# Kernel tuning notes

Hardware: AMD Instinct MI355X
Metric: run time of the kernel (lower is better)

## Reference

```python
import jax, jax.numpy as jnp
import numpy as np

B, D, C = 4096, 4096, 1024


def setup_inputs() -> dict:
    key = jax.random.key(0)
    kx, kw = jax.random.split(key)
    x = jax.random.normal(kx, (B, D), dtype=jnp.float32)
    # kaiming_normal_ with nonlinearity='relu': std = sqrt(2 / fan_in)
    W = jax.random.normal(kw, (C, D), dtype=jnp.float32) * jnp.sqrt(2.0 / D)
    return {"x": x, "W": W}


def reference(x, W):
    # Original: -( (x[:, :, None] - W.T[None, :, :])**2 ).mean(axis=1)
    d = x.shape[1]
    x_sq = jnp.sum(x * x, axis=1, keepdims=True)        # [B, 1]
    w_sq = jnp.sum(W * W, axis=1)[None, :]              # [1, C]
    cross = jnp.einsum('bd,cd->bc', x, W)               # [B, C] tensor-core GEMM
    return -(x_sq - 2.0 * cross + w_sq) / d
```

## Files before the change

kernel.cpp:

```cpp
#include <hip/hip_runtime.h>
#include <hip/hip_bf16.h>


typedef float f32x4 __attribute__((ext_vector_type(4)));
typedef float f32x2 __attribute__((ext_vector_type(2)));
typedef float f32x16 __attribute__((ext_vector_type(16)));
typedef int i32x4 __attribute__((ext_vector_type(4)));
typedef int i32x8 __attribute__((ext_vector_type(8)));

#define BDIM 4096
#define DDIM 4096
#define CDIM 1024
#define TM 128
#define TN 128
#define BK 64
#define NIT (DDIM / BK)
#define SCALE 32.0f
#define INV_SS (1.0f/1024.0f)

#define WAITV(N) asm volatile("s_waitcnt vmcnt(" #N ")" ::: "memory")

__global__ __launch_bounds__(256) void cvt_rowsq(
    const float* __restrict__ x, const float* __restrict__ W,
    unsigned char* __restrict__ xb, unsigned char* __restrict__ wb,
    float* __restrict__ xsq, float* __restrict__ wsq)
{
    const int lane = threadIdx.x & 63;
    const int row = blockIdx.x * 4 + (threadIdx.x >> 6);

    const float* src;
    unsigned char* dst;
    float* sq;
    if (row < BDIM) {
        src = x + (size_t)row * DDIM;
        dst = xb + (size_t)row * DDIM;
        sq = xsq + row;
    } else {
        int r = row - BDIM;
        src = W + (size_t)r * DDIM;
        dst = wb + (size_t)r * DDIM;
        sq = wsq + r;
    }

    const float4* s4 = (const float4*)src;
    unsigned int* d4 = (unsigned int*)dst;
    float a = 0.f;
    #pragma unroll
    for (int s = 0; s < DDIM / 4 / 64; ++s) {
        float4 f = s4[lane + 64 * s];
        a += f.x * f.x + f.y * f.y + f.z * f.z + f.w * f.w;
        unsigned int p = 0;
        p = __builtin_amdgcn_cvt_pk_fp8_f32(f.x * SCALE, f.y * SCALE, p, false);
        p = __builtin_amdgcn_cvt_pk_fp8_f32(f.z * SCALE, f.w * SCALE, p, true);
        d4[lane + 64 * s] = p;
    }
    #pragma unroll
    for (int off = 32; off > 0; off >>= 1) a += __shfl_down(a, off);
    if (lane == 0) *sq = a;
}


__device__ __forceinline__ i32x8 cat8(i32x4 lo, i32x4 hi) {
    return __builtin_shufflevector(lo, hi, 0, 1, 2, 3, 4, 5, 6, 7);
}

#define MXMFMA(A, Bv, C)                                                  \
    __builtin_amdgcn_mfma_scale_f32_32x32x64_f8f6f4(                      \
        (A), (Bv), (C), 0, 0, 0, 0x7F7F7F7F, 0, 0x7F7F7F7F)

#define GLOAD16(gp, lp)                                                   \
    __builtin_amdgcn_global_load_lds(                                     \
        (const __attribute__((address_space(1))) void*)(gp),              \
        (__attribute__((address_space(3))) void*)(lp), 16, 0, 0)

__global__ __launch_bounds__(256) void gemm_eucl(
    const unsigned char* __restrict__ xb,
    const unsigned char* __restrict__ wb,
    const float* __restrict__ xsq, const float* __restrict__ wsq,
    float* __restrict__ out)
{
    __shared__ unsigned char sm[4 * 3 * 8192];

    const int tid = threadIdx.x;
    const int lane = tid & 63;
    const int w = tid >> 6;
    const int wr = w >> 1;
    const int wc = w & 1;
    const int bm = blockIdx.x * TM;
    const int bn = blockIdx.y * TN;

    unsigned char* wbase = sm + w * 24576;

    const int lr = lane >> 2;
    const int schunk = ((lane & 3) ^ ((lane >> 3) & 3)) * 16;
    const unsigned char* gA[4];
    const unsigned char* gB[4];
    #pragma unroll
    for (int i = 0; i < 4; ++i) {
        gA[i] = xb + (size_t)(bm + wr * 64 + 16 * i + lr) * DDIM + schunk;
        gB[i] = wb + (size_t)(bn + wc * 64 + 16 * i + lr) * DDIM + schunk;
    }

#define STAGE(q, t)                                                       \
    do {                                                                  \
        _Pragma("unroll")                                                 \
        for (int i = 0; i < 4; ++i) {                                     \
            GLOAD16(gA[i] + (t) * BK, wbase + (q) * 8192 + i * 1024);     \
            GLOAD16(gB[i] + (t) * BK, wbase + (q) * 8192 + 4096 + i * 1024); \
        }                                                                 \
    } while (0)

    const int s_rd = ((lane & 31) >> 1) & 3;
    const int c0s = ((lane >> 5) * 2) ^ s_rd;
    const unsigned char* aR0 = wbase + (lane & 31) * 64 + c0s * 16;
    const unsigned char* aR1 = wbase + (lane & 31) * 64 + (c0s ^ 1) * 16;
    const unsigned char* bR0 = aR0 + 4096;
    const unsigned char* bR1 = aR1 + 4096;

    f32x16 acc[4] = {};

#define COMPUTE(qo)                                                       \
    do {                                                                  \
        i32x8 fb0 = cat8(*(const i32x4*)(bR0 + (qo)),                     \
                         *(const i32x4*)(bR1 + (qo)));                    \
        i32x8 fb1 = cat8(*(const i32x4*)(bR0 + (qo) + 2048),              \
                         *(const i32x4*)(bR1 + (qo) + 2048));             \
        i32x8 fa0 = cat8(*(const i32x4*)(aR0 + (qo)),                     \
                         *(const i32x4*)(aR1 + (qo)));                    \
        i32x8 fa1 = cat8(*(const i32x4*)(aR0 + (qo) + 2048),              \
                         *(const i32x4*)(aR1 + (qo) + 2048));             \
        __builtin_amdgcn_s_setprio(1);                                    \
        acc[0] = MXMFMA(fa0, fb0, acc[0]);                                \
        acc[1] = MXMFMA(fa0, fb1, acc[1]);                                \
        acc[2] = MXMFMA(fa1, fb0, acc[2]);                                \
        acc[3] = MXMFMA(fa1, fb1, acc[3]);                                \
        __builtin_amdgcn_s_setprio(0);                                    \
    } while (0)

    STAGE(0, 0);
    STAGE(1, 1);

    #pragma unroll 6
    for (int t = 0; t < 60; ++t) {
        WAITV(8);
        STAGE((t + 2) % 3, t + 2);
        COMPUTE((t % 3) * 8192);
    }
    WAITV(8); STAGE(2, 62); COMPUTE(0 * 8192);
    WAITV(8); STAGE(0, 63); COMPUTE(1 * 8192);
    WAITV(8); COMPUTE(2 * 8192);
    WAITV(0); COMPUTE(0 * 8192);

    const float c1m = 2.0f * INV_SS / (float)DDIM;
    const float c2 = 1.0f / (float)DDIM;
    const int gn0 = bn + wc * 64 + (lane & 31);
    const int gm_b = bm + wr * 64 + (lane >> 5) * 4;
    const float wv0 = wsq[gn0];
    const float wv1 = wsq[gn0 + 32];
    #pragma unroll
    for (int i = 0; i < 2; ++i)
        #pragma unroll
        for (int g = 0; g < 4; ++g)
            #pragma unroll
            for (int r = 0; r < 4; ++r) {
                const int gm = gm_b + i * 32 + g * 8 + r;
                const float xs = xsq[gm];
                out[(size_t)gm * CDIM + gn0] =
                    acc[i * 2 + 0][g * 4 + r] * c1m - (xs + wv0) * c2;
                out[(size_t)gm * CDIM + gn0 + 32] =
                    acc[i * 2 + 1][g * 4 + r] * c1m - (xs + wv1) * c2;
            }
#undef STAGE
#undef COMPUTE
}

__global__ void fallback_kernel(const float* __restrict__ x, const float* __restrict__ W,
                                float* __restrict__ out)
{
    int c = blockIdx.x * blockDim.x + threadIdx.x;
    int b = blockIdx.y;
    if (c >= CDIM) return;
    const float* xr = x + (size_t)b * DDIM;
    const float* wr = W + (size_t)c * DDIM;
    float xs = 0.f, ws = 0.f, cr = 0.f;
    for (int d = 0; d < DDIM; ++d) {
        float xv = xr[d], wv = wr[d];
        xs += xv * xv; ws += wv * wv; cr += xv * wv;
    }
    out[(size_t)b * CDIM + c] = (2.0f * cr - xs - ws) / (float)DDIM;
}

extern "C" void kernel_launch(void* const* d_in, const int* in_sizes, int n_in,
                              void* d_out, int out_size, void* d_ws, size_t ws_size,
                              hipStream_t stream) {
    const float* x = (const float*)d_in[0];
    const float* W = (const float*)d_in[1];
    float* out = (float*)d_out;

    size_t need = (size_t)(BDIM + CDIM) * DDIM
                + (size_t)(BDIM + CDIM) * sizeof(float);
    if (ws_size < need) {
        fallback_kernel<<<dim3(CDIM / 256, BDIM), 256, 0, stream>>>(x, W, out);
        return;
    }

    unsigned char* xb = (unsigned char*)d_ws;
    unsigned char* wb = xb + (size_t)BDIM * DDIM;
    float* xsq = (float*)(wb + (size_t)CDIM * DDIM);
    float* wsq = xsq + BDIM;

    cvt_rowsq<<<(BDIM + CDIM) / 4, 256, 0, stream>>>(x, W, xb, wb, xsq, wsq);
    gemm_eucl<<<dim3(BDIM / TM, CDIM / TN), 256, 0, stream>>>(xb, wb, xsq, wsq, out);
}
```

Before: 136.1 us.

## Pre-tile FP8 operands into MFMA fragment layout and load straight to registers

The conversion kernel now writes FP8 data in a fragment-major layout, so each 32-row tile is stored as per-lane 32-byte chunks for every 64-wide K step. The GEMM drops the LDS staging path and instead loads fragments directly from global memory into registers, using a three-deep register ring buffer to overlap loads with MFMAs. This removes LDS traffic and swizzling, at the cost of no data reuse across waves: each wave fetches its own A and B fragments from global or L2. It also uses more registers and depends on the vmcnt wait counts being right.

```diff
diff --git a/kernel.cpp b/kernel.cpp
--- a/kernel.cpp
+++ b/kernel.cpp
@@ -29,31 +29,43 @@
     const int row = blockIdx.x * 4 + (threadIdx.x >> 6);
 
     const float* src;
-    unsigned char* dst;
+    unsigned char* dstb;
     float* sq;
+    int r;
     if (row < BDIM) {
         src = x + (size_t)row * DDIM;
-        dst = xb + (size_t)row * DDIM;
+        dstb = xb; r = row;
         sq = xsq + row;
     } else {
-        int r = row - BDIM;
+        r = row - BDIM;
         src = W + (size_t)r * DDIM;
-        dst = wb + (size_t)r * DDIM;
+        dstb = wb;
         sq = wsq + r;
     }
 
     const float4* s4 = (const float4*)src;
-    unsigned int* d4 = (unsigned int*)dst;
     float a = 0.f;
-    #pragma unroll
-    for (int s = 0; s < DDIM / 4 / 64; ++s) {
-        float4 f = s4[lane + 64 * s];
+    unsigned int pk[16];
+    #pragma unroll
+    for (int u = 0; u < 16; ++u) {
+        float4 f = s4[lane * 16 + u];
         a += f.x * f.x + f.y * f.y + f.z * f.z + f.w * f.w;
         unsigned int p = 0;
         p = __builtin_amdgcn_cvt_pk_fp8_f32(f.x * SCALE, f.y * SCALE, p, false);
         p = __builtin_amdgcn_cvt_pk_fp8_f32(f.z * SCALE, f.w * SCALE, p, true);
-        d4[lane + 64 * s] = p;
-    }
+        pk[u] = p;
+    }
+    unsigned char* db = dstb + (size_t)(r >> 5) * 131072
+                      + (size_t)lane * 2048 + (r & 31) * 32;
+    i32x4 v0 = {(int)pk[0], (int)pk[1], (int)pk[2], (int)pk[3]};
+    i32x4 v1 = {(int)pk[4], (int)pk[5], (int)pk[6], (int)pk[7]};
+    i32x4 v2 = {(int)pk[8], (int)pk[9], (int)pk[10], (int)pk[11]};
+    i32x4 v3 = {(int)pk[12], (int)pk[13], (int)pk[14], (int)pk[15]};
+    *(i32x4*)(db)        = v0;
+    *(i32x4*)(db + 16)   = v1;
+    *(i32x4*)(db + 1024) = v2;
+    *(i32x4*)(db + 1040) = v3;
+
     #pragma unroll
     for (int off = 32; off > 0; off >>= 1) a += __shfl_down(a, off);
     if (lane == 0) *sq = a;
@@ -68,10 +80,7 @@
     __builtin_amdgcn_mfma_scale_f32_32x32x64_f8f6f4(                      \
         (A), (Bv), (C), 0, 0, 0, 0x7F7F7F7F, 0, 0x7F7F7F7F)
 
-#define GLOAD16(gp, lp)                                                   \
-    __builtin_amdgcn_global_load_lds(                                     \
-        (const __attribute__((address_space(1))) void*)(gp),              \
-        (__attribute__((address_space(3))) void*)(lp), 16, 0, 0)
+struct FragS { i32x4 a0l, a0h, a1l, a1h, b0l, b0h, b1l, b1h; };
 
 __global__ __launch_bounds__(256) void gemm_eucl(
     const unsigned char* __restrict__ xb,
@@ -79,8 +88,6 @@
     const float* __restrict__ xsq, const float* __restrict__ wsq,
     float* __restrict__ out)
 {
-    __shared__ unsigned char sm[4 * 3 * 8192];
-
     const int tid = threadIdx.x;
     const int lane = tid & 63;
     const int w = tid >> 6;
@@ -89,67 +96,53 @@
     const int bm = blockIdx.x * TM;
     const int bn = blockIdx.y * TN;
 
-    unsigned char* wbase = sm + w * 24576;
-
-    const int lr = lane >> 2;
-    const int schunk = ((lane & 3) ^ ((lane >> 3) & 3)) * 16;
-    const unsigned char* gA[4];
-    const unsigned char* gB[4];
-    #pragma unroll
-    for (int i = 0; i < 4; ++i) {
-        gA[i] = xb + (size_t)(bm + wr * 64 + 16 * i + lr) * DDIM + schunk;
-        gB[i] = wb + (size_t)(bn + wc * 64 + 16 * i + lr) * DDIM + schunk;
-    }
-
-#define STAGE(q, t)                                                       \
+    const int mt0 = (bm >> 5) + wr * 2;
+    const int nt0 = (bn >> 5) + wc * 2;
+    const unsigned char* pA0 = xb + (size_t)(mt0 + 0) * 131072 + (size_t)lane * 32;
+    const unsigned char* pA1 = xb + (size_t)(mt0 + 1) * 131072 + (size_t)lane * 32;
+    const unsigned char* pB0 = wb + (size_t)(nt0 + 0) * 131072 + (size_t)lane * 32;
+    const unsigned char* pB1 = wb + (size_t)(nt0 + 1) * 131072 + (size_t)lane * 32;
+
+#define LOADF(S, t)                                                       \
     do {                                                                  \
-        _Pragma("unroll")                                                 \
-        for (int i = 0; i < 4; ++i) {                                     \
-            GLOAD16(gA[i] + (t) * BK, wbase + (q) * 8192 + i * 1024);     \
-            GLOAD16(gB[i] + (t) * BK, wbase + (q) * 8192 + 4096 + i * 1024); \
-        }                                                                 \
+        (S).a0l = *(const i32x4*)(pA0 + (size_t)(t) * 2048);              \
+        (S).a0h = *(const i32x4*)(pA0 + (size_t)(t) * 2048 + 16);         \
+        (S).a1l = *(const i32x4*)(pA1 + (size_t)(t) * 2048);              \
+        (S).a1h = *(const i32x4*)(pA1 + (size_t)(t) * 2048 + 16);         \
+        (S).b0l = *(const i32x4*)(pB0 + (size_t)(t) * 2048);              \
+        (S).b0h = *(const i32x4*)(pB0 + (size_t)(t) * 2048 + 16);         \
+        (S).b1l = *(const i32x4*)(pB1 + (size_t)(t) * 2048);              \
+        (S).b1h = *(const i32x4*)(pB1 + (size_t)(t) * 2048 + 16);         \
     } while (0)
 
-    const int s_rd = ((lane & 31) >> 1) & 3;
-    const int c0s = ((lane >> 5) * 2) ^ s_rd;
-    const unsigned char* aR0 = wbase + (lane & 31) * 64 + c0s * 16;
-    const unsigned char* aR1 = wbase + (lane & 31) * 64 + (c0s ^ 1) * 16;
-    const unsigned char* bR0 = aR0 + 4096;
-    const unsigned char* bR1 = aR1 + 4096;
-
     f32x16 acc[4] = {};
 
-#define COMPUTE(qo)                                                       \
+#define COMPUTE(S)                                                        \
     do {                                                                  \
-        i32x8 fb0 = cat8(*(const i32x4*)(bR0 + (qo)),                     \
-                         *(const i32x4*)(bR1 + (qo)));                    \
-        i32x8 fb1 = cat8(*(const i32x4*)(bR0 + (qo) + 2048),              \
-                         *(const i32x4*)(bR1 + (qo) + 2048));             \
-        i32x8 fa0 = cat8(*(const i32x4*)(aR0 + (qo)),                     \
-                         *(const i32x4*)(aR1 + (qo)));                    \
-        i32x8 fa1 = cat8(*(const i32x4*)(aR0 + (qo) + 2048),              \
-                         *(const i32x4*)(aR1 + (qo) + 2048));             \
-        __builtin_amdgcn_s_setprio(1);                                    \
+        i32x8 fa0 = cat8((S).a0l, (S).a0h);                               \
+        i32x8 fa1 = cat8((S).a1l, (S).a1h);                               \
+        i32x8 fb0 = cat8((S).b0l, (S).b0h);                               \
+        i32x8 fb1 = cat8((S).b1l, (S).b1h);                               \
         acc[0] = MXMFMA(fa0, fb0, acc[0]);                                \
         acc[1] = MXMFMA(fa0, fb1, acc[1]);                                \
         acc[2] = MXMFMA(fa1, fb0, acc[2]);                                \
         acc[3] = MXMFMA(fa1, fb1, acc[3]);                                \
-        __builtin_amdgcn_s_setprio(0);                                    \
     } while (0)
 
-    STAGE(0, 0);
-    STAGE(1, 1);
-
-    #pragma unroll 6
-    for (int t = 0; t < 60; ++t) {
-        WAITV(8);
-        STAGE((t + 2) % 3, t + 2);
-        COMPUTE((t % 3) * 8192);
-    }
-    WAITV(8); STAGE(2, 62); COMPUTE(0 * 8192);
-    WAITV(8); STAGE(0, 63); COMPUTE(1 * 8192);
-    WAITV(8); COMPUTE(2 * 8192);
-    WAITV(0); COMPUTE(0 * 8192);
+    FragS S[3];
+    LOADF(S[0], 0);
+    LOADF(S[1], 1);
+    LOADF(S[2], 2);
+
+    #pragma unroll
+    for (int t = 0; t < NIT - 3; ++t) {
+        WAITV(16);
+        COMPUTE(S[t % 3]);
+        LOADF(S[t % 3], t + 3);
+    }
+    WAITV(16); COMPUTE(S[1]);
+    WAITV(8);  COMPUTE(S[2]);
+    WAITV(0);  COMPUTE(S[0]);
 
     const float c1m = 2.0f * INV_SS / (float)DDIM;
     const float c2 = 1.0f / (float)DDIM;
@@ -162,15 +155,15 @@
         #pragma unroll
         for (int g = 0; g < 4; ++g)
             #pragma unroll
-            for (int r = 0; r < 4; ++r) {
-                const int gm = gm_b + i * 32 + g * 8 + r;
+            for (int rr = 0; rr < 4; ++rr) {
+                const int gm = gm_b + i * 32 + g * 8 + rr;
                 const float xs = xsq[gm];
                 out[(size_t)gm * CDIM + gn0] =
-                    acc[i * 2 + 0][g * 4 + r] * c1m - (xs + wv0) * c2;
+                    acc[i * 2 + 0][g * 4 + rr] * c1m - (xs + wv0) * c2;
                 out[(size_t)gm * CDIM + gn0 + 32] =
-                    acc[i * 2 + 1][g * 4 + r] * c1m - (xs + wv1) * c2;
+                    acc[i * 2 + 1][g * 4 + rr] * c1m - (xs + wv1) * c2;
             }
-#undef STAGE
+#undef LOADF
 #undef COMPUTE
 }
 
```

Result: no change. 138.5 us (+1.7%).

## Share LDS tiles across waves with BK=128 and a 4-stage barrier pipeline

Applied to the files above, without the earlier changes.

Each wave previously loaded its own private 64x64 A/B sub-tiles, so rows were duplicated across waves. Now the whole workgroup cooperatively loads 128x128 A/B tiles of depth 128 into shared LDS with an XOR swizzle, and every wave reads its slice from them. A 4-buffer ring with a prefetch distance of two and a workgroup barrier per iteration replaces the per-wave 3-buffer scheme. This halves redundant global/L2 traffic and the iteration count, at the cost of 128KB LDS (lower occupancy) and one barrier per step.

```diff
diff --git a/kernel.cpp b/kernel.cpp
--- a/kernel.cpp
+++ b/kernel.cpp
@@ -13,12 +13,13 @@
 #define CDIM 1024
 #define TM 128
 #define TN 128
-#define BK 64
+#define BK 128
 #define NIT (DDIM / BK)
 #define SCALE 32.0f
 #define INV_SS (1.0f/1024.0f)
 
 #define WAITV(N) asm volatile("s_waitcnt vmcnt(" #N ")" ::: "memory")
+#define BAR()    __builtin_amdgcn_s_barrier()
 
 __global__ __launch_bounds__(256) void cvt_rowsq(
     const float* __restrict__ x, const float* __restrict__ W,
@@ -79,7 +80,7 @@
     const float* __restrict__ xsq, const float* __restrict__ wsq,
     float* __restrict__ out)
 {
-    __shared__ unsigned char sm[4 * 3 * 8192];
+    __shared__ unsigned char sm[4 * 32768];
 
     const int tid = threadIdx.x;
     const int lane = tid & 63;
@@ -89,46 +90,74 @@
     const int bm = blockIdx.x * TM;
     const int bn = blockIdx.y * TN;
 
-    unsigned char* wbase = sm + w * 24576;
-
-    const int lr = lane >> 2;
-    const int schunk = ((lane & 3) ^ ((lane >> 3) & 3)) * 16;
+    const int sr = tid >> 3;
+    const int sc = ((tid & 7) ^ ((tid >> 3) & 7)) * 16;
     const unsigned char* gA[4];
     const unsigned char* gB[4];
     #pragma unroll
     for (int i = 0; i < 4; ++i) {
-        gA[i] = xb + (size_t)(bm + wr * 64 + 16 * i + lr) * DDIM + schunk;
-        gB[i] = wb + (size_t)(bn + wc * 64 + 16 * i + lr) * DDIM + schunk;
+        gA[i] = xb + (size_t)(bm + i * 32 + sr) * DDIM + sc;
+        gB[i] = wb + (size_t)(bn + i * 32 + sr) * DDIM + sc;
     }
 
 #define STAGE(q, t)                                                       \
     do {                                                                  \
         _Pragma("unroll")                                                 \
-        for (int i = 0; i < 4; ++i) {                                     \
-            GLOAD16(gA[i] + (t) * BK, wbase + (q) * 8192 + i * 1024);     \
-            GLOAD16(gB[i] + (t) * BK, wbase + (q) * 8192 + 4096 + i * 1024); \
-        }                                                                 \
+        for (int i = 0; i < 4; ++i)                                       \
+            GLOAD16(gA[i] + (size_t)(t) * BK,                             \
+                    sm + (q) * 32768 + i * 4096 + w * 1024);              \
+        _Pragma("unroll")                                                 \
+        for (int i = 0; i < 4; ++i)                                       \
+            GLOAD16(gB[i] + (size_t)(t) * BK,                             \
+                    sm + (q) * 32768 + 16384 + i * 4096 + w * 1024);      \
     } while (0)
 
-    const int s_rd = ((lane & 31) >> 1) & 3;
-    const int c0s = ((lane >> 5) * 2) ^ s_rd;
-    const unsigned char* aR0 = wbase + (lane & 31) * 64 + c0s * 16;
-    const unsigned char* aR1 = wbase + (lane & 31) * 64 + (c0s ^ 1) * 16;
-    const unsigned char* bR0 = aR0 + 4096;
-    const unsigned char* bR1 = aR1 + 4096;
+    const int rl = lane & 31;
+    const int sw = lane & 7;
+    const int kb = (lane >> 5) * 2;
+    const int rowA = (wr * 64 + rl) * BK;
+    const int rowB = (wc * 64 + rl) * BK;
+    const int sl00 = (kb ^ sw) * 16;
+    const int sl01 = ((kb + 1) ^ sw) * 16;
+    const int sl10 = ((kb + 4) ^ sw) * 16;
+    const int sl11 = ((kb + 5) ^ sw) * 16;
+    const unsigned char* aP00 = sm + rowA + sl00;
+    const unsigned char* aP01 = sm + rowA + sl01;
+    const unsigned char* aP10 = sm + rowA + sl10;
+    const unsigned char* aP11 = sm + rowA + sl11;
+    const unsigned char* bP00 = sm + 16384 + rowB + sl00;
+    const unsigned char* bP01 = sm + 16384 + rowB + sl01;
+    const unsigned char* bP10 = sm + 16384 + rowB + sl10;
+    const unsigned char* bP11 = sm + 16384 + rowB + sl11;
 
     f32x16 acc[4] = {};
 
 #define COMPUTE(qo)                                                       \
     do {                                                                  \
-        i32x8 fb0 = cat8(*(const i32x4*)(bR0 + (qo)),                     \
-                         *(const i32x4*)(bR1 + (qo)));                    \
-        i32x8 fb1 = cat8(*(const i32x4*)(bR0 + (qo) + 2048),              \
-                         *(const i32x4*)(bR1 + (qo) + 2048));             \
-        i32x8 fa0 = cat8(*(const i32x4*)(aR0 + (qo)),                     \
-                         *(const i32x4*)(aR1 + (qo)));                    \
-        i32x8 fa1 = cat8(*(const i32x4*)(aR0 + (qo) + 2048),              \
-                         *(const i32x4*)(aR1 + (qo) + 2048));             \
+                                                             \
+        i32x8 fb0 = cat8(*(const i32x4*)(bP00 + (qo)),                    \
+                         *(const i32x4*)(bP01 + (qo)));                   \
+        i32x8 fb1 = cat8(*(const i32x4*)(bP00 + (qo) + 4096),             \
+                         *(const i32x4*)(bP01 + (qo) + 4096));            \
+        i32x8 fa0 = cat8(*(const i32x4*)(aP00 + (qo)),                    \
+                         *(const i32x4*)(aP01 + (qo)));                   \
+        i32x8 fa1 = cat8(*(const i32x4*)(aP00 + (qo) + 4096),             \
+                         *(const i32x4*)(aP01 + (qo) + 4096));            \
+        __builtin_amdgcn_s_setprio(1);                                    \
+        acc[0] = MXMFMA(fa0, fb0, acc[0]);                                \
+        acc[1] = MXMFMA(fa0, fb1, acc[1]);                                \
+        acc[2] = MXMFMA(fa1, fb0, acc[2]);                                \
+        acc[3] = MXMFMA(fa1, fb1, acc[3]);                                \
+        __builtin_amdgcn_s_setprio(0);                                    \
+                                                             \
+        fb0 = cat8(*(const i32x4*)(bP10 + (qo)),                          \
+                   *(const i32x4*)(bP11 + (qo)));                         \
+        fb1 = cat8(*(const i32x4*)(bP10 + (qo) + 4096),                   \
+                   *(const i32x4*)(bP11 + (qo) + 4096));                  \
+        fa0 = cat8(*(const i32x4*)(aP10 + (qo)),                          \
+                   *(const i32x4*)(aP11 + (qo)));                         \
+        fa1 = cat8(*(const i32x4*)(aP10 + (qo) + 4096),                   \
+                   *(const i32x4*)(aP11 + (qo) + 4096));                  \
         __builtin_amdgcn_s_setprio(1);                                    \
         acc[0] = MXMFMA(fa0, fb0, acc[0]);                                \
         acc[1] = MXMFMA(fa0, fb1, acc[1]);                                \
@@ -140,16 +169,15 @@
     STAGE(0, 0);
     STAGE(1, 1);
 
-    #pragma unroll 6
-    for (int t = 0; t < 60; ++t) {
-        WAITV(8);
-        STAGE((t + 2) % 3, t + 2);
-        COMPUTE((t % 3) * 8192);
-    }
-    WAITV(8); STAGE(2, 62); COMPUTE(0 * 8192);
-    WAITV(8); STAGE(0, 63); COMPUTE(1 * 8192);
-    WAITV(8); COMPUTE(2 * 8192);
-    WAITV(0); COMPUTE(0 * 8192);
+    #pragma unroll 4
+    for (int t = 0; t < NIT - 2; ++t) {
+        STAGE((t + 2) & 3, t + 2);
+        WAITV(16);
+        BAR();
+        COMPUTE((t & 3) * 32768);
+    }
+    WAITV(8); BAR(); COMPUTE(((NIT - 2) & 3) * 32768);
+    WAITV(0); BAR(); COMPUTE(((NIT - 1) & 3) * 32768);
 
     const float c1m = 2.0f * INV_SS / (float)DDIM;
     const float c2 = 1.0f / (float)DDIM;
```

After: 133.7 us. Within noise of the previous version (-1.8%).
